# Kernel tuning notes

Hardware: AMD Instinct MI355X
Metric: run time of the kernel (lower is better)

## Reference

```python
import math
import jax, jax.numpy as jnp
import numpy as np


def kaiser_sinc_filter1d(cutoff, half_width, kernel_size):
    even = kernel_size % 2 == 0
    half_size = kernel_size // 2
    delta_f = 4 * half_width
    A = 2.285 * (half_size - 1) * math.pi * delta_f + 7.95
    if A > 50.0:
        beta = 0.1102 * (A - 8.7)
    elif A >= 21.0:
        beta = 0.5842 * (A - 21) ** 0.4 + 0.07886 * (A - 21.0)
    else:
        beta = 0.0
    window = np.kaiser(kernel_size, beta)  # == torch.kaiser_window(periodic=False)
    if even:
        time = np.arange(-half_size, half_size) + 0.5
    else:
        time = np.arange(kernel_size) - half_size
    if cutoff == 0:
        filt = np.zeros_like(time)
    else:
        filt = 2 * cutoff * window * np.sinc(2 * cutoff * time)
        filt = filt / filt.sum()
    return jnp.asarray(filt, dtype=jnp.float32)  # [K]


def _depthwise_conv1d(x, filt, stride, lhs_dilation, padding):
    # x: [B, C, T]; filt: [K] shared across channels (groups=C depthwise)
    C = x.shape[1]
    K = filt.shape[0]
    w = jnp.broadcast_to(filt.reshape(1, 1, K), (C, 1, K))
    return jax.lax.conv_general_dilated(
        x, w,
        window_strides=(stride,),
        padding=[padding],
        lhs_dilation=(lhs_dilation,),
        dimension_numbers=("NCH", "OIH", "NCH"),
        feature_group_count=C,
    )


UP = 2
DOWN = 2
UP_K = 12
DOWN_K = 12


def setup_inputs() -> dict:
    key = jax.random.key(0)
    B, C, T = 16, 512, 4096
    x = jax.random.normal(key, (B, C, T), dtype=jnp.float32)
    alpha = jnp.zeros((1, C, 1), dtype=jnp.float32)
    beta = jnp.zeros((1, C, 1), dtype=jnp.float32)
    up_filter = kaiser_sinc_filter1d(0.5 / UP, 0.6 / UP, UP_K)
    down_filter = kaiser_sinc_filter1d(0.5 / DOWN, 0.6 / DOWN, DOWN_K)
    return {"x": x, "alpha": alpha, "beta": beta,
            "up_filter": up_filter, "down_filter": down_filter}


def reference(x, alpha, beta, up_filter, down_filter):
    # ---- UpSample1d(ratio=UP, kernel_size=UP_K) ----
    pad = UP_K // UP - 1
    pad_left = pad * UP + (UP_K - UP) // 2
    pad_right = pad * UP + (UP_K - UP + 1) // 2
    xp = jnp.pad(x, ((0, 0), (0, 0), (pad, pad)), mode="edge")  # replicate pad
    # conv_transpose1d(stride=UP) == conv with lhs_dilation=UP, full padding, flipped kernel
    y = UP * _depthwise_conv1d(xp, up_filter[::-1], stride=1,
                               lhs_dilation=UP, padding=(UP_K - 1, UP_K - 1))
    y = y[..., pad_left:-pad_right]  # [B, C, UP*T]

    # ---- SnakeBeta ----
    y = y + 1.0 / (jnp.exp(beta) + 1e-9) * jnp.square(jnp.sin(y * jnp.exp(alpha)))

    # ---- DownSample1d(ratio=DOWN, kernel_size=DOWN_K) via LowPassFilter1d ----
    even = DOWN_K % 2 == 0
    dpl = DOWN_K // 2 - int(even)
    dpr = DOWN_K // 2
    yp = jnp.pad(y, ((0, 0), (0, 0), (dpl, dpr)), mode="edge")
    out = _depthwise_conv1d(yp, down_filter, stride=DOWN,
                            lhs_dilation=1, padding=(0, 0))  # [B, C, T]
    return out
```

## Files before the change

kernel.cpp:

```cpp
#include <hip/hip_runtime.h>
#include <math.h>


#define T_LEN 4096
#define NT    256
#define W     16

__global__ __launch_bounds__(NT, 2) void aa_act_kernel(
    const float* __restrict__ x,
    const float* __restrict__ alpha,
    const float* __restrict__ beta,
    const float* __restrict__ upf,
    const float* __restrict__ downf,
    float* __restrict__ out,
    int C)
{
    const int t   = threadIdx.x;
    const int row = blockIdx.x;
    const int c   = row % C;
    const int o0  = t * W;

    const float* __restrict__ xr = x + (size_t)row * T_LEN;
    float* __restrict__ outr     = out + (size_t)row * T_LEN;

    float ue[6], uo[6], d[12];
#pragma unroll
    for (int m = 0; m < 6; ++m) {
        ue[m] = 2.0f * upf[11 - 2 * m];
        uo[m] = 2.0f * upf[10 - 2 * m];
    }
#pragma unroll
    for (int i = 0; i < 12; ++i) d[i] = downf[i];

    const float ea = __expf(alpha[c]);
    const float rb = 1.0f / (__expf(beta[c]) + 1e-9f);

    const bool lo = (t == 0);
    const bool hi = (t == NT - 1);

    float f[32];
    if (!lo && !hi) {
        const float4* p = (const float4*)(xr + o0 - 8);
#pragma unroll
        for (int i = 0; i < 8; ++i) ((float4*)f)[i] = p[i];
    } else {
#pragma unroll
        for (int i = 0; i < 32; ++i)
            f[i] = xr[min(max(o0 - 8 + i, 0), T_LEN - 1)];
    }

    float acc[W];
#pragma unroll
    for (int r = 0; r < W; ++r) acc[r] = 0.0f;

    float Rv = 0.0f;

#pragma unroll
    for (int i = 0; i < 21; ++i) {
        float ye = f[i + 3] * ue[0];
        ye = fmaf(f[i + 4], ue[1], ye);
        ye = fmaf(f[i + 5], ue[2], ye);
        ye = fmaf(f[i + 6], ue[3], ye);
        ye = fmaf(f[i + 7], ue[4], ye);
        ye = fmaf(f[i + 8], ue[5], ye);
        float yo = f[i + 3] * uo[0];
        yo = fmaf(f[i + 4], uo[1], yo);
        yo = fmaf(f[i + 5], uo[2], yo);
        yo = fmaf(f[i + 6], uo[3], yo);
        yo = fmaf(f[i + 7], uo[4], yo);
        yo = fmaf(f[i + 8], uo[5], yo);
        float se = __sinf(ye * ea);
        float so = __sinf(yo * ea);
        float ev = fmaf(rb * se, se, ye);
        float ov = fmaf(rb * so, so, yo);

        if (i == 18) {
            if (hi) { Rv = ov; ev = ov; }
        }
        if (i >= 19) {
            if (hi) { ev = Rv; ov = Rv; }
        }
        if (i == 2) {
            if (lo) {
                acc[0] = fmaf(ev, d[0] + d[1] + d[2] + d[3], acc[0]);
                acc[1] = fmaf(ev, d[0] + d[1], acc[1]);
                ov = ev;
            }
        }

        const int rlo = (i - 5 > 0) ? (i - 5) : 0;
        const int rhi = (i < W - 1) ? i : (W - 1);
        if (i < 2) {
            if (!lo) {
#pragma unroll
                for (int r = rlo; r <= rhi; ++r)
                    acc[r] = fmaf(ev, d[2 * (i - r) + 1],
                             fmaf(ov, d[2 * (i - r)], acc[r]));
            }
        } else {
#pragma unroll
            for (int r = rlo; r <= rhi; ++r)
                acc[r] = fmaf(ev, d[2 * (i - r) + 1],
                         fmaf(ov, d[2 * (i - r)], acc[r]));
        }
    }

#pragma unroll
    for (int i = 0; i < 4; ++i)
        ((float4*)(outr + o0))[i] = *(float4*)(acc + 4 * i);
}

extern "C" void kernel_launch(void* const* d_in, const int* in_sizes, int n_in,
                              void* d_out, int out_size, void* d_ws, size_t ws_size,
                              hipStream_t stream) {
    const float* x     = (const float*)d_in[0];
    const float* alpha = (const float*)d_in[1];
    const float* beta  = (const float*)d_in[2];
    const float* upf   = (const float*)d_in[3];
    const float* downf = (const float*)d_in[4];
    float* out = (float*)d_out;

    const int C    = in_sizes[1];
    const int rows = in_sizes[0] / T_LEN;

    dim3 grid(rows), block(NT);
    hipLaunchKernelGGL(aa_act_kernel, grid, block, 0, stream,
                       x, alpha, beta, upf, downf, out, C);
}
```

Before: 282.6 us.

## Stage input and output rows through swizzled LDS for coalesced global access

Loads each row cooperatively into shared memory with coalesced float4 reads, including edge clamping, then has threads read their 32-sample windows from an XOR-swizzled LDS layout. The outputs are written back through LDS so global stores are consecutive float4s across threads. Launch bounds are raised to 4 blocks per CU. Previously each thread issued strided 64-byte chunks directly to global memory. The change adds barriers and about 16KB of LDS per block, which may limit occupancy.

```diff
diff --git a/kernel.cpp b/kernel.cpp
--- a/kernel.cpp
+++ b/kernel.cpp
@@ -5,8 +5,13 @@
 #define T_LEN 4096
 #define NT    256
 #define W     16
+#define LDSF  4112
+#define NQ_IN 1028
+#define NQ_OUT 1024
 
-__global__ __launch_bounds__(NT, 2) void aa_act_kernel(
+#define SWZ(b) ((b) ^ ((((b) >> 7) & 7) << 4))
+
+__global__ __launch_bounds__(NT, 4) void aa_act_kernel(
     const float* __restrict__ x,
     const float* __restrict__ alpha,
     const float* __restrict__ beta,
@@ -15,10 +20,11 @@
     float* __restrict__ out,
     int C)
 {
+    __shared__ __align__(16) float sx[LDSF];
+
     const int t   = threadIdx.x;
     const int row = blockIdx.x;
     const int c   = row % C;
-    const int o0  = t * W;
 
     const float* __restrict__ xr = x + (size_t)row * T_LEN;
     float* __restrict__ outr     = out + (size_t)row * T_LEN;
@@ -38,15 +44,27 @@
     const bool lo = (t == 0);
     const bool hi = (t == NT - 1);
 
+    for (int q = t; q < NQ_IN; q += NT) {
+        const int gi = 4 * q - 8;
+        float4 v;
+        if (gi >= 0 && gi <= T_LEN - 4) {
+            v = *(const float4*)(xr + gi);
+        } else {
+            v.x = xr[min(max(gi + 0, 0), T_LEN - 1)];
+            v.y = xr[min(max(gi + 1, 0), T_LEN - 1)];
+            v.z = xr[min(max(gi + 2, 0), T_LEN - 1)];
+            v.w = xr[min(max(gi + 3, 0), T_LEN - 1)];
+        }
+        *(float4*)((char*)sx + SWZ(16 * q)) = v;
+    }
+    __syncthreads();
+
     float f[32];
-    if (!lo && !hi) {
-        const float4* p = (const float4*)(xr + o0 - 8);
 #pragma unroll
-        for (int i = 0; i < 8; ++i) ((float4*)f)[i] = p[i];
-    } else {
-#pragma unroll
-        for (int i = 0; i < 32; ++i)
-            f[i] = xr[min(max(o0 - 8 + i, 0), T_LEN - 1)];
+    for (int i = 0; i < 8; ++i) {
+        float4 v = *(const float4*)((const char*)sx + SWZ(64 * t + 16 * i));
+        f[4 * i + 0] = v.x; f[4 * i + 1] = v.y;
+        f[4 * i + 2] = v.z; f[4 * i + 3] = v.w;
     }
 
     float acc[W];
@@ -105,9 +123,18 @@
         }
     }
 
+    __syncthreads();
 #pragma unroll
     for (int i = 0; i < 4; ++i)
-        ((float4*)(outr + o0))[i] = *(float4*)(acc + 4 * i);
+        *(float4*)((char*)sx + SWZ(64 * t + 16 * i)) =
+            make_float4(acc[4 * i + 0], acc[4 * i + 1],
+                        acc[4 * i + 2], acc[4 * i + 3]);
+    __syncthreads();
+
+    for (int q = t; q < NQ_OUT; q += NT) {
+        float4 v = *(const float4*)((const char*)sx + SWZ(16 * q));
+        ((float4*)outr)[q] = v;
+    }
 }
 
 extern "C" void kernel_launch(void* const* d_in, const int* in_sizes, int n_in,
```

Result: faster. 242.6 us (-14.1%).
